# Kernel tuning notes

Hardware: AMD Instinct MI355X
Metric: run time of the kernel (lower is better)

The kernel has to match this reference:

```python
import jax, jax.numpy as jnp
import numpy as np

B, I, O, G = 4096, 256, 256, 8
GRID_MIN, GRID_MAX, RHO = -2.0, 2.0, 1.0


def setup_inputs() -> dict:
    key = jax.random.key(0)
    ks = jax.random.split(key, 8)
    return {
        "x_re": jax.random.normal(ks[0], (B, I), dtype=jnp.float32),
        "x_im": jax.random.normal(ks[1], (B, I), dtype=jnp.float32),
        "realweights": jax.random.normal(ks[2], (I, O, G, G), dtype=jnp.float32),
        "complexweights": jax.random.normal(ks[3], (I, O, G, G), dtype=jnp.float32),
        "silu_weight_re": jax.random.normal(ks[4], (I, O), dtype=jnp.float32),
        "silu_weight_im": jax.random.normal(ks[5], (I, O), dtype=jnp.float32),
        "silu_bias_re": 0.1 * jax.random.normal(ks[6], (I, O), dtype=jnp.float32),
        "silu_bias_im": 0.1 * jax.random.normal(ks[7], (I, O), dtype=jnp.float32),
    }


def reference(x_re, x_im, realweights, complexweights,
              silu_weight_re, silu_weight_im, silu_bias_re, silu_bias_im):
    # Complex grid: grid[u, v] = lin[u] + i * lin[v]
    lin = jnp.linspace(GRID_MIN, GRID_MAX, G, dtype=x_re.dtype)
    # |x - grid|^2 = (x_re - lin_u)^2 + (x_im - lin_v)^2  -> (B, I, G, G)
    dre = x_re[:, :, None, None] - lin[None, None, :, None]
    dim = x_im[:, :, None, None] - lin[None, None, None, :]
    basis = jnp.exp(-(dre * dre + dim * dim) / RHO)  # real-valued (B, I, G, G)
    # RBF contraction: real and imaginary output channels
    out_re = jnp.einsum('biuv,iouv->bo', basis, realweights)
    out_im = jnp.einsum('biuv,iouv->bo', basis, complexweights)
    # Complex SiLU (complex_weight variant): silu applied component-wise,
    # then complex-multiplied by silu_weight, plus bias, summed over i.
    s_re = jax.nn.silu(x_re)  # (B, I)
    s_im = jax.nn.silu(x_im)
    out_re = out_re + s_re @ silu_weight_re - s_im @ silu_weight_im + jnp.sum(silu_bias_re, axis=0)
    out_im = out_im + s_im @ silu_weight_re + s_re @ silu_weight_im + jnp.sum(silu_bias_im, axis=0)
    # Return complex output as stacked (real, imag): (B, O, 2)
    return jnp.stack([out_re, out_im], axis=-1)
```

## Files before the change

kernel.cpp:

```cpp
#include <hip/hip_runtime.h>
#include <hip/hip_fp16.h>
#include <stdint.h>

typedef float floatx4 __attribute__((ext_vector_type(4)));
typedef short short8 __attribute__((ext_vector_type(8)));

constexpr int I_SZ = 256, O_SZ = 256, NCOL = 512, B_SZ = 4096;
constexpr int KSTEPS = 264;
constexpr float GSTEP = 4.0f / 7.0f;
constexpr float NLOG2E = -1.44269504088896f;

__device__ __forceinline__ uint32_t pk_bf16(float lo, float hi) {
  return __builtin_amdgcn_perm(__float_as_uint(hi), __float_as_uint(lo), 0x07060302u);
}
__device__ __forceinline__ short rne_bf16(float f) {
  uint32_t u = __float_as_uint(f);
  return (short)((u + 0x7FFFu + ((u >> 16) & 1u)) >> 16);
}

__device__ __forceinline__ void gload_lds16(const void* g, void* l) {
  __builtin_amdgcn_global_load_lds((const __attribute__((address_space(1))) void*)g,
                                   (__attribute__((address_space(3))) void*)l,
                                   16, 0, 0);
}

__device__ __forceinline__ float silu_f(float a) {
  return a * __builtin_amdgcn_rcpf(1.f + __builtin_amdgcn_exp2f(a * NLOG2E));
}

__global__ void pack_weights(const float* __restrict__ rw, const float* __restrict__ cw,
                             const float* __restrict__ swre, const float* __restrict__ swim,
                             short* __restrict__ wpack) {
  int idx = blockIdx.x * 256 + threadIdx.x;
  int kb = idx >> 12;
  int rem = idx & 4095;
  int n = rem >> 3, gp = rem & 7;
  int g = gp ^ (n & 7);
  int o = n >> 1, c = n & 1;
  float w[8];
  if (kb < 256) {
    const float* W = (c ? cw : rw) + (((size_t)kb * O_SZ + o) << 6) + (g << 3);
    float4 a = *(const float4*)W;
    float4 b = *(const float4*)(W + 4);
    w[0] = a.x; w[1] = a.y; w[2] = a.z; w[3] = a.w;
    w[4] = b.x; w[5] = b.y; w[6] = b.z; w[7] = b.w;
  } else {
    int kp0 = ((kb - 256) << 6) + (g << 3);
    #pragma unroll
    for (int e = 0; e < 8; ++e) {
      int kp = kp0 + e, i = kp >> 1, ci = kp & 1;
      float a = swre[i * O_SZ + o], b = swim[i * O_SZ + o];
      w[e] = (c == 0) ? (ci == 0 ? a : -b) : (ci == 0 ? b : a);
    }
  }
  uint32_t h[8];
  #pragma unroll
  for (int e = 0; e < 8; ++e) h[e] = (uint32_t)(uint16_t)rne_bf16(w[e]);
  uint4 val = make_uint4(h[0] | (h[1] << 16), h[2] | (h[3] << 16),
                         h[4] | (h[5] << 16), h[6] | (h[7] << 16));
  *(uint4*)(wpack + (size_t)idx * 8) = val;
}

__global__ void transpose_x(const float* __restrict__ xre, const float* __restrict__ xim,
                            __half* __restrict__ xT) {
  __shared__ float tile[64][65];
  int bt = blockIdx.x & 63;
  int it = (blockIdx.x >> 6) & 3;
  int c  = blockIdx.x >> 8;
  const float* src = (c ? xim : xre);
  int b0 = bt << 6, i0 = it << 6;
  int t = threadIdx.x;
  int il = t & 63, bh = t >> 6;
  #pragma unroll
  for (int k = 0; k < 16; ++k) {
    int bl = bh + (k << 2);
    tile[bl][il] = src[(size_t)(b0 + bl) * I_SZ + i0 + il];
  }
  __syncthreads();
  int bl2 = t & 63, ih = t >> 6;
  __half* dst = xT + ((size_t)c * I_SZ + i0) * B_SZ + b0;
  #pragma unroll
  for (int k = 0; k < 16; ++k) {
    int il2 = ih + (k << 2);
    dst[(size_t)il2 * B_SZ + bl2] = __float2half(tile[bl2][il2]);
  }
}

__global__ void bias_sums(const float* __restrict__ bre, const float* __restrict__ bim,
                          float* __restrict__ bsum) {
  int n = blockIdx.x, o = n >> 1, l = threadIdx.x;
  const float* src = ((n & 1) ? bim : bre) + o;
  float s = 0.f;
  #pragma unroll
  for (int a = 0; a < 4; ++a) s += src[(size_t)(a * 64 + l) * O_SZ];
  #pragma unroll
  for (int off = 32; off; off >>= 1) s += __shfl_down(s, off, 64);
  if (l == 0) bsum[n] = s;
}

__global__ __launch_bounds__(256, 4) void cvkan_gemm(
    const float* __restrict__ xre, const float* __restrict__ xim,
    const __half* __restrict__ xT,
    const short* __restrict__ wpack, const float* __restrict__ bsum,
    float* __restrict__ out) {
  __shared__ __align__(16) short Bs[128 * 64];
  __shared__ __align__(16) short As[128 * 64];

  const int tid = threadIdx.x;
  const int bid = blockIdx.x;
  const int kch = bid & 7;
  const int mn = bid >> 3;
  const int mt = mn >> 2, nt = mn & 3;
  const int b0 = mt * 128, n0 = nt * 128;
  const int l = tid & 63, w = tid >> 6;
  const int wr = w >> 1, wc = w & 1;
  const int lm = l & 15, q = l >> 4;
  const int r = tid >> 1, h = tid & 1;

  const __half* xTre = xT;
  const __half* xTim = xT + (size_t)I_SZ * B_SZ;

  floatx4 acc[4][4] = {};

  for (int j = 0; j < 33; ++j) {
    const int s = (j < 32) ? (kch * 32 + j) : (256 + kch);

    float xr = 0.f, xi = 0.f;
    if (j < 32) {
      xr = __half2float(xTre[(size_t)s * B_SZ + b0 + r]);
      xi = __half2float(xTim[(size_t)s * B_SZ + b0 + r]);
    }

    {
      const short* src = wpack + (((size_t)s * NCOL + n0) << 6) + (tid << 3);
      short* ldst = Bs + (w << 9);
      gload_lds16(src,        ldst);
      gload_lds16(src + 2048, ldst + 2048);
      gload_lds16(src + 4096, ldst + 4096);
      gload_lds16(src + 6144, ldst + 6144);
    }

    if (j < 32) {
      float eiv[8];
      #pragma unroll
      for (int v = 0; v < 8; ++v) {
        float d = xi - (-2.0f + v * GSTEP);
        eiv[v] = __builtin_amdgcn_exp2f(d * d * NLOG2E);
      }
      #pragma unroll
      for (int uu = 0; uu < 4; ++uu) {
        int u = h * 4 + uu;
        float d = xr - (-2.0f + u * GSTEP);
        float er = __builtin_amdgcn_exp2f(d * d * NLOG2E);
        uint4 val = make_uint4(pk_bf16(er * eiv[0], er * eiv[1]),
                               pk_bf16(er * eiv[2], er * eiv[3]),
                               pk_bf16(er * eiv[4], er * eiv[5]),
                               pk_bf16(er * eiv[6], er * eiv[7]));
        *(uint4*)(As + (r << 6) + ((u ^ (r & 7)) << 3)) = val;
      }
    } else {
      int sl = kch;
      #pragma unroll
      for (int gg = 0; gg < 4; ++gg) {
        int g = h * 4 + gg;
        const float* pr = xre + (size_t)(b0 + r) * I_SZ + (sl << 5) + (g << 2);
        const float* pi = xim + (size_t)(b0 + r) * I_SZ + (sl << 5) + (g << 2);
        uint4 val = make_uint4(pk_bf16(silu_f(pr[0]), silu_f(pi[0])),
                               pk_bf16(silu_f(pr[1]), silu_f(pi[1])),
                               pk_bf16(silu_f(pr[2]), silu_f(pi[2])),
                               pk_bf16(silu_f(pr[3]), silu_f(pi[3])));
        *(uint4*)(As + (r << 6) + ((g ^ (r & 7)) << 3)) = val;
      }
    }

    __builtin_amdgcn_s_waitcnt(0);
    __syncthreads();

    short8 bf[4][2];
    #pragma unroll
    for (int nn = 0; nn < 4; ++nn) {
      int col = wc * 64 + nn * 16 + lm;
      const short* bp = Bs + (col << 6);
      bf[nn][0] = *(const short8*)(bp + ((q       ^ (col & 7)) << 3));
      bf[nn][1] = *(const short8*)(bp + (((q + 4) ^ (col & 7)) << 3));
    }
    #pragma unroll
    for (int mm = 0; mm < 4; ++mm) {
      int row = wr * 64 + mm * 16 + lm;
      const short* ap = As + (row << 6);
      short8 a0 = *(const short8*)(ap + ((q       ^ (row & 7)) << 3));
      short8 a1 = *(const short8*)(ap + (((q + 4) ^ (row & 7)) << 3));
      #pragma unroll
      for (int nn = 0; nn < 4; ++nn) {
        acc[mm][nn] = __builtin_amdgcn_mfma_f32_16x16x32_bf16(a0, bf[nn][0], acc[mm][nn], 0, 0, 0);
        acc[mm][nn] = __builtin_amdgcn_mfma_f32_16x16x32_bf16(a1, bf[nn][1], acc[mm][nn], 0, 0, 0);
      }
    }
    __syncthreads();
  }

  #pragma unroll
  for (int nn = 0; nn < 4; ++nn) {
    int col = n0 + wc * 64 + nn * 16 + lm;
    float bv = (kch == 7) ? bsum[col] : 0.0f;
    #pragma unroll
    for (int mm = 0; mm < 4; ++mm) {
      int row0 = b0 + wr * 64 + mm * 16 + (q << 2);
      #pragma unroll
      for (int r2 = 0; r2 < 4; ++r2)
        atomicAdd(out + (size_t)(row0 + r2) * NCOL + col, acc[mm][nn][r2] + bv);
    }
  }
}

extern "C" void kernel_launch(void* const* d_in, const int* in_sizes, int n_in,
                              void* d_out, int out_size, void* d_ws, size_t ws_size,
                              hipStream_t stream) {
  const float* xre  = (const float*)d_in[0];
  const float* xim  = (const float*)d_in[1];
  const float* rw   = (const float*)d_in[2];
  const float* cw   = (const float*)d_in[3];
  const float* swre = (const float*)d_in[4];
  const float* swim = (const float*)d_in[5];
  const float* bre  = (const float*)d_in[6];
  const float* bim  = (const float*)d_in[7];
  float* out = (float*)d_out;

  size_t wpack_bytes = (size_t)KSTEPS * NCOL * 64 * 2;
  short* wpack = (short*)d_ws;
  float* bsum  = (float*)((char*)d_ws + wpack_bytes);
  __half* xT   = (__half*)((char*)d_ws + wpack_bytes + 2048);

  hipMemsetAsync(d_out, 0, (size_t)B_SZ * NCOL * sizeof(float), stream);
  pack_weights<<<(KSTEPS * NCOL * 8) / 256, 256, 0, stream>>>(rw, cw, swre, swim, wpack);
  transpose_x<<<512, 256, 0, stream>>>(xre, xim, xT);
  bias_sums<<<NCOL, 64, 0, stream>>>(bre, bim, bsum);
  cvkan_gemm<<<1024, 256, 0, stream>>>(xre, xim, xT, wpack, bsum, out);
}
```

Baseline: 205.9 us.

## Drop LDS staging in GEMM, load fragments directly to registers, fuse prelude kernels

Result: slower. 352.8 us (+71.3%).

```diff
diff --git a/kernel.cpp b/kernel.cpp
--- a/kernel.cpp
+++ b/kernel.cpp
@@ -17,198 +17,176 @@
   uint32_t u = __float_as_uint(f);
   return (short)((u + 0x7FFFu + ((u >> 16) & 1u)) >> 16);
 }
-
-__device__ __forceinline__ void gload_lds16(const void* g, void* l) {
-  __builtin_amdgcn_global_load_lds((const __attribute__((address_space(1))) void*)g,
-                                   (__attribute__((address_space(3))) void*)l,
-                                   16, 0, 0);
-}
-
 __device__ __forceinline__ float silu_f(float a) {
   return a * __builtin_amdgcn_rcpf(1.f + __builtin_amdgcn_exp2f(a * NLOG2E));
 }
 
-__global__ void pack_weights(const float* __restrict__ rw, const float* __restrict__ cw,
-                             const float* __restrict__ swre, const float* __restrict__ swim,
-                             short* __restrict__ wpack) {
-  int idx = blockIdx.x * 256 + threadIdx.x;
-  int kb = idx >> 12;
-  int rem = idx & 4095;
-  int n = rem >> 3, gp = rem & 7;
-  int g = gp ^ (n & 7);
-  int o = n >> 1, c = n & 1;
-  float w[8];
-  if (kb < 256) {
-    const float* W = (c ? cw : rw) + (((size_t)kb * O_SZ + o) << 6) + (g << 3);
-    float4 a = *(const float4*)W;
-    float4 b = *(const float4*)(W + 4);
-    w[0] = a.x; w[1] = a.y; w[2] = a.z; w[3] = a.w;
-    w[4] = b.x; w[5] = b.y; w[6] = b.z; w[7] = b.w;
+__global__ void prelude(const float* __restrict__ rw, const float* __restrict__ cw,
+                        const float* __restrict__ swre, const float* __restrict__ swim,
+                        const float* __restrict__ bre, const float* __restrict__ bim,
+                        const float* __restrict__ xre, const float* __restrict__ xim,
+                        short* __restrict__ wpack, float* __restrict__ bsum,
+                        __half* __restrict__ xT) {
+  __shared__ float tile[64][65];
+  const int bid = blockIdx.x, tid = threadIdx.x;
+
+  if (bid < 4224) {
+    int idx = bid * 256 + tid;
+    int kb = idx >> 12;
+    int rem = idx & 4095;
+    int n = rem >> 3, g = rem & 7;
+    int o = n >> 1, c = n & 1;
+    float w[8];
+    if (kb < 256) {
+      const float* W = (c ? cw : rw) + ((((size_t)kb * O_SZ + o) << 3) + g << 3);
+      float4 a = *(const float4*)W;
+      float4 b = *(const float4*)(W + 4);
+      w[0] = a.x; w[1] = a.y; w[2] = a.z; w[3] = a.w;
+      w[4] = b.x; w[5] = b.y; w[6] = b.z; w[7] = b.w;
+    } else {
+      int kp0 = ((kb - 256) << 6) + (g << 3);
+      #pragma unroll
+      for (int e = 0; e < 8; ++e) {
+        int kp = kp0 + e, i = kp >> 1, ci = kp & 1;
+        float a = swre[i * O_SZ + o], b = swim[i * O_SZ + o];
+        w[e] = (c == 0) ? (ci == 0 ? a : -b) : (ci == 0 ? b : a);
+      }
+    }
+    uint32_t h[8];
+    #pragma unroll
+    for (int e = 0; e < 8; ++e) h[e] = (uint32_t)(uint16_t)rne_bf16(w[e]);
+    uint4 val = make_uint4(h[0] | (h[1] << 16), h[2] | (h[3] << 16),
+                           h[4] | (h[5] << 16), h[6] | (h[7] << 16));
+    *(uint4*)(wpack + (size_t)idx * 8) = val;
+  } else if (bid < 4736) {
+    int tb = bid - 4224;
+    int bt = tb & 63, it = (tb >> 6) & 3, c = tb >> 8;
+    const float* src = (c ? xim : xre);
+    int b0 = bt << 6, i0 = it << 6;
+    int il = tid & 63, bh = tid >> 6;
+    #pragma unroll
+    for (int k = 0; k < 16; ++k) {
+      int bl = bh + (k << 2);
+      tile[bl][il] = src[(size_t)(b0 + bl) * I_SZ + i0 + il];
+    }
+    __syncthreads();
+    int bl2 = tid & 63, ih = tid >> 6;
+    __half* dst = xT + ((size_t)c * I_SZ + i0) * B_SZ + b0;
+    #pragma unroll
+    for (int k = 0; k < 16; ++k) {
+      int il2 = ih + (k << 2);
+      dst[(size_t)il2 * B_SZ + bl2] = __float2half(tile[bl2][il2]);
+    }
   } else {
-    int kp0 = ((kb - 256) << 6) + (g << 3);
-    #pragma unroll
-    for (int e = 0; e < 8; ++e) {
-      int kp = kp0 + e, i = kp >> 1, ci = kp & 1;
-      float a = swre[i * O_SZ + o], b = swim[i * O_SZ + o];
-      w[e] = (c == 0) ? (ci == 0 ? a : -b) : (ci == 0 ? b : a);
-    }
+    int w = tid >> 6, l = tid & 63;
+    int n = (bid - 4736) * 4 + w;
+    int o = n >> 1;
+    const float* src = ((n & 1) ? bim : bre) + o;
+    float s = 0.f;
+    #pragma unroll
+    for (int a = 0; a < 4; ++a) s += src[(size_t)(a * 64 + l) * O_SZ];
+    #pragma unroll
+    for (int off = 32; off; off >>= 1) s += __shfl_down(s, off, 64);
+    if (l == 0) bsum[n] = s;
   }
-  uint32_t h[8];
-  #pragma unroll
-  for (int e = 0; e < 8; ++e) h[e] = (uint32_t)(uint16_t)rne_bf16(w[e]);
-  uint4 val = make_uint4(h[0] | (h[1] << 16), h[2] | (h[3] << 16),
-                         h[4] | (h[5] << 16), h[6] | (h[7] << 16));
-  *(uint4*)(wpack + (size_t)idx * 8) = val;
-}
-
-__global__ void transpose_x(const float* __restrict__ xre, const float* __restrict__ xim,
-                            __half* __restrict__ xT) {
-  __shared__ float tile[64][65];
-  int bt = blockIdx.x & 63;
-  int it = (blockIdx.x >> 6) & 3;
-  int c  = blockIdx.x >> 8;
-  const float* src = (c ? xim : xre);
-  int b0 = bt << 6, i0 = it << 6;
-  int t = threadIdx.x;
-  int il = t & 63, bh = t >> 6;
-  #pragma unroll
-  for (int k = 0; k < 16; ++k) {
-    int bl = bh + (k << 2);
-    tile[bl][il] = src[(size_t)(b0 + bl) * I_SZ + i0 + il];
-  }
-  __syncthreads();
-  int bl2 = t & 63, ih = t >> 6;
-  __half* dst = xT + ((size_t)c * I_SZ + i0) * B_SZ + b0;
-  #pragma unroll
-  for (int k = 0; k < 16; ++k) {
-    int il2 = ih + (k << 2);
-    dst[(size_t)il2 * B_SZ + bl2] = __float2half(tile[bl2][il2]);
-  }
-}
-
-__global__ void bias_sums(const float* __restrict__ bre, const float* __restrict__ bim,
-                          float* __restrict__ bsum) {
-  int n = blockIdx.x, o = n >> 1, l = threadIdx.x;
-  const float* src = ((n & 1) ? bim : bre) + o;
-  float s = 0.f;
-  #pragma unroll
-  for (int a = 0; a < 4; ++a) s += src[(size_t)(a * 64 + l) * O_SZ];
-  #pragma unroll
-  for (int off = 32; off; off >>= 1) s += __shfl_down(s, off, 64);
-  if (l == 0) bsum[n] = s;
-}
-
-__global__ __launch_bounds__(256, 4) void cvkan_gemm(
+}
+
+__global__ __launch_bounds__(256, 2) void cvkan_gemm(
     const float* __restrict__ xre, const float* __restrict__ xim,
     const __half* __restrict__ xT,
     const short* __restrict__ wpack, const float* __restrict__ bsum,
     float* __restrict__ out) {
-  __shared__ __align__(16) short Bs[128 * 64];
-  __shared__ __align__(16) short As[128 * 64];
-
-  const int tid = threadIdx.x;
-  const int bid = blockIdx.x;
+  const int tid = threadIdx.x, bid = blockIdx.x;
   const int kch = bid & 7;
   const int mn = bid >> 3;
   const int mt = mn >> 2, nt = mn & 3;
   const int b0 = mt * 128, n0 = nt * 128;
-  const int l = tid & 63, w = tid >> 6;
-  const int wr = w >> 1, wc = w & 1;
+  const int w = tid >> 6, l = tid & 63;
   const int lm = l & 15, q = l >> 4;
-  const int r = tid >> 1, h = tid & 1;
+  const int row0 = b0 + w * 32 + lm;
 
   const __half* xTre = xT;
   const __half* xTim = xT + (size_t)I_SZ * B_SZ;
 
-  floatx4 acc[4][4] = {};
+  floatx4 acc[2][8] = {};
 
   for (int j = 0; j < 33; ++j) {
     const int s = (j < 32) ? (kch * 32 + j) : (256 + kch);
 
-    float xr = 0.f, xi = 0.f;
+    const short* bbase = wpack + ((size_t)s * NCOL + n0) * 64 + (q << 3);
+    short8 bf[8][2];
+    #pragma unroll
+    for (int nn = 0; nn < 8; ++nn) {
+      const short* p = bbase + ((nn * 16 + lm) << 6);
+      bf[nn][0] = *(const short8*)p;
+      bf[nn][1] = *(const short8*)(p + 32);
+    }
+
+    short8 af[2][2];
     if (j < 32) {
-      xr = __half2float(xTre[(size_t)s * B_SZ + b0 + r]);
-      xi = __half2float(xTim[(size_t)s * B_SZ + b0 + r]);
-    }
-
-    {
-      const short* src = wpack + (((size_t)s * NCOL + n0) << 6) + (tid << 3);
-      short* ldst = Bs + (w << 9);
-      gload_lds16(src,        ldst);
-      gload_lds16(src + 2048, ldst + 2048);
-      gload_lds16(src + 4096, ldst + 4096);
-      gload_lds16(src + 6144, ldst + 6144);
-    }
-
-    if (j < 32) {
-      float eiv[8];
-      #pragma unroll
-      for (int v = 0; v < 8; ++v) {
-        float d = xi - (-2.0f + v * GSTEP);
-        eiv[v] = __builtin_amdgcn_exp2f(d * d * NLOG2E);
-      }
-      #pragma unroll
-      for (int uu = 0; uu < 4; ++uu) {
-        int u = h * 4 + uu;
-        float d = xr - (-2.0f + u * GSTEP);
-        float er = __builtin_amdgcn_exp2f(d * d * NLOG2E);
-        uint4 val = make_uint4(pk_bf16(er * eiv[0], er * eiv[1]),
-                               pk_bf16(er * eiv[2], er * eiv[3]),
-                               pk_bf16(er * eiv[4], er * eiv[5]),
-                               pk_bf16(er * eiv[6], er * eiv[7]));
-        *(uint4*)(As + (r << 6) + ((u ^ (r & 7)) << 3)) = val;
+      #pragma unroll
+      for (int mm = 0; mm < 2; ++mm) {
+        const int row = row0 + mm * 16;
+        float xr = __half2float(xTre[(size_t)s * B_SZ + row]);
+        float xi = __half2float(xTim[(size_t)s * B_SZ + row]);
+        float eiv[8];
+        #pragma unroll
+        for (int v = 0; v < 8; ++v) {
+          float d = xi - (-2.0f + v * GSTEP);
+          eiv[v] = __builtin_amdgcn_exp2f(d * d * NLOG2E);
+        }
+        float d0 = xr - (-2.0f + q * GSTEP);
+        float d1 = xr - (-2.0f + (q + 4) * GSTEP);
+        float er0 = __builtin_amdgcn_exp2f(d0 * d0 * NLOG2E);
+        float er1 = __builtin_amdgcn_exp2f(d1 * d1 * NLOG2E);
+        union { short8 v; uint32_t u[4]; } a0, a1;
+        #pragma unroll
+        for (int t = 0; t < 4; ++t) {
+          a0.u[t] = pk_bf16(er0 * eiv[2 * t], er0 * eiv[2 * t + 1]);
+          a1.u[t] = pk_bf16(er1 * eiv[2 * t], er1 * eiv[2 * t + 1]);
+        }
+        af[mm][0] = a0.v;
+        af[mm][1] = a1.v;
       }
     } else {
-      int sl = kch;
-      #pragma unroll
-      for (int gg = 0; gg < 4; ++gg) {
-        int g = h * 4 + gg;
-        const float* pr = xre + (size_t)(b0 + r) * I_SZ + (sl << 5) + (g << 2);
-        const float* pi = xim + (size_t)(b0 + r) * I_SZ + (sl << 5) + (g << 2);
-        uint4 val = make_uint4(pk_bf16(silu_f(pr[0]), silu_f(pi[0])),
-                               pk_bf16(silu_f(pr[1]), silu_f(pi[1])),
-                               pk_bf16(silu_f(pr[2]), silu_f(pi[2])),
-                               pk_bf16(silu_f(pr[3]), silu_f(pi[3])));
-        *(uint4*)(As + (r << 6) + ((g ^ (r & 7)) << 3)) = val;
-      }
-    }
-
-    __builtin_amdgcn_s_waitcnt(0);
-    __syncthreads();
-
-    short8 bf[4][2];
-    #pragma unroll
-    for (int nn = 0; nn < 4; ++nn) {
-      int col = wc * 64 + nn * 16 + lm;
-      const short* bp = Bs + (col << 6);
-      bf[nn][0] = *(const short8*)(bp + ((q       ^ (col & 7)) << 3));
-      bf[nn][1] = *(const short8*)(bp + (((q + 4) ^ (col & 7)) << 3));
-    }
-    #pragma unroll
-    for (int mm = 0; mm < 4; ++mm) {
-      int row = wr * 64 + mm * 16 + lm;
-      const short* ap = As + (row << 6);
-      short8 a0 = *(const short8*)(ap + ((q       ^ (row & 7)) << 3));
-      short8 a1 = *(const short8*)(ap + (((q + 4) ^ (row & 7)) << 3));
-      #pragma unroll
-      for (int nn = 0; nn < 4; ++nn) {
-        acc[mm][nn] = __builtin_amdgcn_mfma_f32_16x16x32_bf16(a0, bf[nn][0], acc[mm][nn], 0, 0, 0);
-        acc[mm][nn] = __builtin_amdgcn_mfma_f32_16x16x32_bf16(a1, bf[nn][1], acc[mm][nn], 0, 0, 0);
-      }
-    }
-    __syncthreads();
+      const int sl = kch;
+      #pragma unroll
+      for (int mm = 0; mm < 2; ++mm) {
+        const int row = row0 + mm * 16;
+        #pragma unroll
+        for (int kh = 0; kh < 2; ++kh) {
+          int i0 = sl * 32 + (q + kh * 4) * 4;
+          float4 fr = *(const float4*)(xre + (size_t)row * I_SZ + i0);
+          float4 fi = *(const float4*)(xim + (size_t)row * I_SZ + i0);
+          union { short8 v; uint32_t u[4]; } a;
+          a.u[0] = pk_bf16(silu_f(fr.x), silu_f(fi.x));
+          a.u[1] = pk_bf16(silu_f(fr.y), silu_f(fi.y));
+          a.u[2] = pk_bf16(silu_f(fr.z), silu_f(fi.z));
+          a.u[3] = pk_bf16(silu_f(fr.w), silu_f(fi.w));
+          af[mm][kh] = a.v;
+        }
+      }
+    }
+
+    #pragma unroll
+    for (int mm = 0; mm < 2; ++mm)
+      #pragma unroll
+      for (int nn = 0; nn < 8; ++nn) {
+        acc[mm][nn] = __builtin_amdgcn_mfma_f32_16x16x32_bf16(af[mm][0], bf[nn][0], acc[mm][nn], 0, 0, 0);
+        acc[mm][nn] = __builtin_amdgcn_mfma_f32_16x16x32_bf16(af[mm][1], bf[nn][1], acc[mm][nn], 0, 0, 0);
+      }
   }
 
   #pragma unroll
-  for (int nn = 0; nn < 4; ++nn) {
-    int col = n0 + wc * 64 + nn * 16 + lm;
+  for (int nn = 0; nn < 8; ++nn) {
+    int col = n0 + nn * 16 + lm;
     float bv = (kch == 7) ? bsum[col] : 0.0f;
     #pragma unroll
-    for (int mm = 0; mm < 4; ++mm) {
-      int row0 = b0 + wr * 64 + mm * 16 + (q << 2);
+    for (int mm = 0; mm < 2; ++mm) {
+      int r0 = b0 + w * 32 + mm * 16 + (q << 2);
       #pragma unroll
       for (int r2 = 0; r2 < 4; ++r2)
-        atomicAdd(out + (size_t)(row0 + r2) * NCOL + col, acc[mm][nn][r2] + bv);
+        atomicAdd(out + (size_t)(r0 + r2) * NCOL + col, acc[mm][nn][r2] + bv);
     }
   }
 }
@@ -229,11 +207,9 @@
   size_t wpack_bytes = (size_t)KSTEPS * NCOL * 64 * 2;
   short* wpack = (short*)d_ws;
   float* bsum  = (float*)((char*)d_ws + wpack_bytes);
-  __half* xT   = (__half*)((char*)d_ws + wpack_bytes + 2048);
+  __half* xT   = (__half*)((char*)d_ws + wpack_bytes + 4096);
 
   hipMemsetAsync(d_out, 0, (size_t)B_SZ * NCOL * sizeof(float), stream);
-  pack_weights<<<(KSTEPS * NCOL * 8) / 256, 256, 0, stream>>>(rw, cw, swre, swim, wpack);
-  transpose_x<<<512, 256, 0, stream>>>(xre, xim, xT);
-  bias_sums<<<NCOL, 64, 0, stream>>>(bre, bim, bsum);
+  prelude<<<4864, 256, 0, stream>>>(rw, cw, swre, swim, bre, bim, xre, xim, wpack, bsum, xT);
   cvkan_gemm<<<1024, 256, 0, stream>>>(xre, xim, xT, wpack, bsum, out);
 }
```
